# Performance work log

Measured on AMD Instinct MI355X. Metric: run time of the kernel, lower is better.

The kernel has to match this reference:

```python
import jax, jax.numpy as jnp
import numpy as np

N_QUBITS = 12
N_LAYERS = 2
PATCH = 16
NPS = 14  # patches per side for 224/16
N_PATCHES = NPS * NPS
SCALE = 1.0 / np.sqrt(N_QUBITS)


def _butterfly_gates(n):
    # Faithful replication of QuantumOrthogonalLayer.butterfly_circuit indexing:
    # param_idx increments even when the (idx1, idx2) pair is skipped.
    gates, pidx = [], 0
    n_bl = int(np.ceil(np.log2(n)))
    for layer in range(n_bl):
        stride = 2 ** layer
        for start in range(0, n - stride, 2 * stride):
            for off in range(stride):
                i1, i2 = start + off, start + off + stride
                if i1 < n and i2 < n:
                    gates.append((pidx, i1, i2))
                pidx += 1
    nppl = sum(2 ** (n_bl - 1 - i) * 2 ** i for i in range(n_bl))  # n_params() = 32
    return gates, nppl

GATES, NPPL = _butterfly_gates(N_QUBITS)

# Pauli-Z sign table: qubit 0 is the most-significant bit of the flattened state index.
_bits = (np.arange(2 ** N_QUBITS)[:, None] >> np.arange(N_QUBITS - 1, -1, -1)[None, :]) & 1
Z_SIGNS = jnp.asarray(1.0 - 2.0 * _bits, dtype=jnp.float32)  # (4096, 12)


def _rbs_u(theta):
    # 4x4 real unitary of RY(2t,w1); CNOT(w1,w2); RY(-2t,w1); CNOT(w1,w2)
    c, s = jnp.cos(theta), jnp.sin(theta)
    c2, s2, cs = c * c, s * s, c * s
    return jnp.stack([
        jnp.stack([c2, s2, -cs, cs]),
        jnp.stack([s2, c2, cs, -cs]),
        jnp.stack([cs, -cs, c2, s2]),
        jnp.stack([-cs, cs, s2, c2]),
    ])


def _apply_2q(state, U, i, j):
    # state: (P, 2, 2, ..., 2); apply U to qubit axes i, j
    st = jnp.moveaxis(state, (1 + i, 1 + j), (-2, -1))
    shp = st.shape
    st = st.reshape(shp[:-2] + (4,)) @ U.T
    return jnp.moveaxis(st.reshape(shp), (-2, -1), (1 + i, 1 + j))


@jax.checkpoint
def quantum_expvals(features, params):
    # features: (P, n_qubits) angles; params: (N_LAYERS * NPPL,)
    P = features.shape[0]
    half = 0.5 * features
    amp = jnp.stack([jnp.cos(half), jnp.sin(half)], axis=-1)  # (P, n, 2) RY(x)|0>
    state = jnp.ones((P, 1), features.dtype)
    for q in range(N_QUBITS):  # product-state angle encoding
        state = (state[:, :, None] * amp[:, q][:, None, :]).reshape(P, -1)
    state = state.reshape((P,) + (2,) * N_QUBITS)
    for l in range(N_LAYERS):
        base = l * NPPL
        for pidx, w1, w2 in GATES:
            state = _apply_2q(state, _rbs_u(params[base + pidx]), w1, w2)
    probs = state.reshape(P, -1) ** 2
    return probs @ Z_SIGNS  # (P, n_qubits) <Z_i>


def setup_inputs() -> dict:
    key = jax.random.key(0)
    ks = jax.random.split(key, 6)
    x = jax.random.normal(ks[0], (4, 3, 224, 224), dtype=jnp.float32)
    W_proj = jax.random.normal(ks[1], (N_QUBITS, PATCH * PATCH), dtype=jnp.float32) / np.sqrt(PATCH * PATCH)
    b_proj = jnp.zeros((N_QUBITS,), jnp.float32)
    q_params = 0.1 * jax.random.normal(ks[2], (N_LAYERS * NPPL,), dtype=jnp.float32)
    k_params = 0.1 * jax.random.normal(ks[3], (N_LAYERS * NPPL,), dtype=jnp.float32)
    v_params = 0.1 * jax.random.normal(ks[4], (N_LAYERS * NPPL,), dtype=jnp.float32)
    W_cls = jax.random.normal(ks[5], (1000, N_PATCHES * N_QUBITS), dtype=jnp.float32) / np.sqrt(N_PATCHES * N_QUBITS)
    b_cls = jnp.zeros((1000,), jnp.float32)
    return {"x": x, "W_proj": W_proj, "b_proj": b_proj, "q_params": q_params,
            "k_params": k_params, "v_params": v_params, "W_cls": W_cls, "b_cls": b_cls}


def reference(x, W_proj, b_proj, q_params, k_params, v_params, W_cls, b_cls):
    B = x.shape[0]
    xg = jnp.mean(x, axis=1)  # channel average -> (B, H, W)
    patches = xg.reshape(B, NPS, PATCH, NPS, PATCH).transpose(0, 1, 3, 2, 4)
    patches = patches.reshape(B, N_PATCHES, PATCH * PATCH)
    proj = patches @ W_proj.T + b_proj  # (B, n_patches, n_qubits)
    feats = proj.reshape(-1, N_QUBITS)
    Q = quantum_expvals(feats, q_params).reshape(B, N_PATCHES, N_QUBITS)
    K = quantum_expvals(feats, k_params).reshape(B, N_PATCHES, N_QUBITS)
    V = quantum_expvals(feats, v_params).reshape(B, N_PATCHES, N_QUBITS)
    attn = jax.nn.softmax(jnp.einsum('bqd,bkd->bqk', Q, K) * SCALE, axis=-1)
    out = jnp.einsum('bqk,bkd->bqd', attn, V)  # (B, n_patches, n_qubits)
    logits = out.reshape(B, -1) @ W_cls.T + b_cls
    return logits
```

## Files before the change

kernel.cpp:

```cpp
#include <hip/hip_runtime.h>
#include <math.h>

#define NQ        12
#define NPS       14
#define NPATCH    196
#define NB        4
#define NCLS      1000
#define FEATDIM   2352
#define SCALE_F   0.28867513459481287f
#define LSTRIDE   33

constexpr int PR[6][5] = {
    {11,10, 9, 8, 7},
    { 7, 6, 5, 4, 3},
    { 3, 2, 1, 0,11},
    {11,10, 7, 6, 3},
    {10, 9, 5, 2, 1},
    { 9, 8, 4, 1, 0},
};
constexpr int PT[6][7] = {
    { 5, 4, 3, 1, 2, 0, 6},
    {11,10, 2, 1, 9, 8, 0},
    { 8, 7, 6, 9, 5, 4,10},
    { 5, 8, 2, 1, 0, 4, 9},
    {11, 7, 8, 4, 6, 3, 0},
    { 5, 3,10, 7, 6, 2,11},
};

constexpr int wgt(int X, int pos) {
    for (int k = 0; k < 5; ++k) if (PR[X][k] == pos) return 1 << k;
    for (int k = 0; k < 7; ++k) if (PT[X][k] == pos) return LSTRIDE << k;
    return 0;
}
constexpr int rimm(int X, int Y, int r) {
    int s = 0;
    for (int j = 0; j < 5; ++j) if ((r >> j) & 1) s += wgt(X, PR[Y][j]);
    return s;
}

template<int X, int Y>
__device__ __forceinline__ void relayout(float amp[32], float* lds, int tid) {
    float* w = lds + LSTRIDE * tid;
    #pragma unroll
    for (int r = 0; r < 32; ++r) w[r] = amp[r];
    __syncthreads();
    int base = 0;
    #pragma unroll
    for (int j = 0; j < 7; ++j)
        base += ((tid >> j) & 1) ? wgt(X, PT[Y][j]) : 0;
    #pragma unroll
    for (int r = 0; r < 32; ++r)
        amp[r] = lds[base + rimm(X, Y, r)];
    __syncthreads();
}

template<int MI, int MJ>
__device__ __forceinline__ void apply_gate(float amp[32], float gc, float gs) {
    #pragma unroll
    for (int m = 0; m < 32; ++m) {
        if (m & (MI | MJ)) continue;
        float a0 = amp[m], a1 = amp[m | MJ], a2 = amp[m | MI], a3 = amp[m | MI | MJ];
        float p  = a0 + a1, q  = a0 - a1;
        float p2 = a2 + a3, q2 = a2 - a3;
        float t1 = 0.5f * p  + gc * q  - gs * q2;
        float t2 = 0.5f * p2 + gc * q2 + gs * q;
        amp[m]           = t1;
        amp[m | MJ]      = p  - t1;
        amp[m | MI]      = t2;
        amp[m | MI | MJ] = p2 - t2;
    }
}

__device__ const int SLOT[12] = {0,3,7,8,4,5,1,9,2,6,10,11};

__global__ __launch_bounds__(128, 4) void qcirc_kernel(
    const float* __restrict__ x,
    const float* __restrict__ Wp,
    const float* __restrict__ bproj,
    const float* __restrict__ qp,
    const float* __restrict__ kp,
    const float* __restrict__ vp,
    float* __restrict__ qkv)
{
    __shared__ __align__(16) float lds[128 * LSTRIDE];
    __shared__ float chs[NQ], shs[NQ];
    __shared__ float gC[40], gS[40];
    __shared__ float red2[2][12];

    const int tid = threadIdx.x;
    const int p = blockIdx.x, b = blockIdx.y, c = blockIdx.z;
    const int bp = b * NPATCH + p;
    const float* params = (c == 0) ? qp : (c == 1) ? kp : vp;

    float part[NQ];
    #pragma unroll
    for (int q = 0; q < NQ; ++q) part[q] = 0.0f;
    {
        int py = p / NPS, px = p % NPS;
        const float* xb = x + (size_t)b * 3 * 224 * 224;
        #pragma unroll
        for (int k = 0; k < 2; ++k) {
            int pix = tid + 128 * k;
            int off = (py * 16 + (pix >> 4)) * 224 + px * 16 + (pix & 15);
            float v = (xb[off] + xb[off + 50176] + xb[off + 100352]) * (1.0f / 3.0f);
            #pragma unroll
            for (int q = 0; q < NQ; ++q) part[q] += v * Wp[q * 256 + pix];
        }
    }
    if (tid < 40) {
        int l = tid / 20, g = tid - l * 20;
        float th = params[l * 32 + g];
        gC[tid] = 0.5f * cosf(2.0f * th);
        gS[tid] = 0.5f * sinf(2.0f * th);
    }
    #pragma unroll
    for (int o = 1; o < 64; o <<= 1) {
        #pragma unroll
        for (int q = 0; q < NQ; ++q) part[q] += __shfl_xor(part[q], o);
    }
    {
        int lane = tid & 63, wv = tid >> 6;
        if (lane == 0) {
            #pragma unroll
            for (int q = 0; q < NQ; ++q) red2[wv][q] = part[q];
        }
    }
    __syncthreads();
    if (tid < NQ) {
        float h = 0.5f * (red2[0][tid] + red2[1][tid] + bproj[tid]);
        chs[tid] = cosf(h); shs[tid] = sinf(h);
    }
    __syncthreads();

    float amp[32];
    {
        float hi = ((tid &  1) ? shs[6]  : chs[6])  *
                   ((tid &  2) ? shs[7]  : chs[7])  *
                   ((tid &  4) ? shs[8]  : chs[8])  *
                   ((tid &  8) ? shs[10] : chs[10]) *
                   ((tid & 16) ? shs[9]  : chs[9])  *
                   ((tid & 32) ? shs[11] : chs[11]) *
                   ((tid & 64) ? shs[5]  : chs[5]);
        float pA[8], pB[4];
        #pragma unroll
        for (int i = 0; i < 8; ++i)
            pA[i] = ((i & 1) ? shs[0] : chs[0]) * ((i & 2) ? shs[1] : chs[1]) *
                    ((i & 4) ? shs[2] : chs[2]);
        #pragma unroll
        for (int i = 0; i < 4; ++i)
            pB[i] = ((i & 1) ? shs[3] : chs[3]) * ((i & 2) ? shs[4] : chs[4]);
        #pragma unroll
        for (int r = 0; r < 32; ++r) amp[r] = pA[r & 7] * pB[r >> 3] * hi;
    }

    #pragma unroll 1
    for (int l = 0; l < 2; ++l) {
        const int bb = l * 20;
        apply_gate<1, 2>(amp, gC[bb+0], gS[bb+0]);
        apply_gate<4, 8>(amp, gC[bb+1], gS[bb+1]);
        apply_gate<1, 4>(amp, gC[bb+6], gS[bb+6]);
        apply_gate<2, 8>(amp, gC[bb+7], gS[bb+7]);
        relayout<0,1>(amp, lds, tid);
        apply_gate<1, 2>(amp, gC[bb+2], gS[bb+2]);
        apply_gate<4, 8>(amp, gC[bb+3], gS[bb+3]);
        apply_gate<1, 4>(amp, gC[bb+8], gS[bb+8]);
        apply_gate<2, 8>(amp, gC[bb+9], gS[bb+9]);
        relayout<1,2>(amp, lds, tid);
        apply_gate<1, 2>(amp, gC[bb+4],  gS[bb+4]);
        apply_gate<4, 8>(amp, gC[bb+5],  gS[bb+5]);
        apply_gate<1, 4>(amp, gC[bb+10], gS[bb+10]);
        apply_gate<2, 8>(amp, gC[bb+11], gS[bb+11]);
        relayout<2,3>(amp, lds, tid);
        apply_gate<1, 4>(amp, gC[bb+12], gS[bb+12]);
        apply_gate<2, 8>(amp, gC[bb+13], gS[bb+13]);
        apply_gate<1,16>(amp, gC[bb+16], gS[bb+16]);
        relayout<3,4>(amp, lds, tid);
        apply_gate<2, 4>(amp, gC[bb+14], gS[bb+14]);
        apply_gate<1, 8>(amp, gC[bb+17], gS[bb+17]);
        relayout<4,5>(amp, lds, tid);
        apply_gate<2, 4>(amp, gC[bb+15], gS[bb+15]);
        apply_gate<1, 8>(amp, gC[bb+18], gS[bb+18]);
        apply_gate<2,16>(amp, gC[bb+19], gS[bb+19]);
        if (l == 0) relayout<5,0>(amp, lds, tid);
    }

    float T, Sq2, Sq3, Sq7, Sq10, Sq11;
    {
        float t1[16]; Sq2 = 0.0f;
        #pragma unroll
        for (int i = 0; i < 16; ++i) {
            float e = amp[2*i] * amp[2*i], o = amp[2*i+1] * amp[2*i+1];
            t1[i] = e + o; Sq2 += e - o;
        }
        float t2[8]; Sq3 = 0.0f;
        #pragma unroll
        for (int i = 0; i < 8; ++i) { t2[i] = t1[2*i] + t1[2*i+1]; Sq3 += t1[2*i] - t1[2*i+1]; }
        float t3[4]; Sq7 = 0.0f;
        #pragma unroll
        for (int i = 0; i < 4; ++i) { t3[i] = t2[2*i] + t2[2*i+1]; Sq7 += t2[2*i] - t2[2*i+1]; }
        float t4[2]; Sq10 = 0.0f;
        #pragma unroll
        for (int i = 0; i < 2; ++i) { t4[i] = t3[2*i] + t3[2*i+1]; Sq10 += t3[2*i] - t3[2*i+1]; }
        T = t4[0] + t4[1]; Sq11 = t4[0] - t4[1];
    }
    float A = T, M[6];
    #pragma unroll
    for (int pbit = 0; pbit < 6; ++pbit) {
        int msk = 1 << pbit;
        float Ap = __shfl_xor(A, msk);
        float d  = A - Ap;
        M[pbit] = (tid & msk) ? -d : d;
        A += Ap;
        #pragma unroll
        for (int k = 0; k < 6; ++k)
            if (k < pbit) M[k] += __shfl_xor(M[k], msk);
        Sq2  += __shfl_xor(Sq2,  msk);
        Sq3  += __shfl_xor(Sq3,  msk);
        Sq7  += __shfl_xor(Sq7,  msk);
        Sq10 += __shfl_xor(Sq10, msk);
        Sq11 += __shfl_xor(Sq11, msk);
    }
    {
        int lane = tid & 63, wv = tid >> 6;
        if (lane == 0) {
            red2[wv][0] = A;
            red2[wv][1] = M[0];
            red2[wv][2] = M[1];
            red2[wv][3] = M[2];
            red2[wv][4] = M[3];
            red2[wv][5] = M[4];
            red2[wv][6] = M[5];
            red2[wv][7] = Sq2;  red2[wv][8]  = Sq3;
            red2[wv][9] = Sq7;  red2[wv][10] = Sq10; red2[wv][11] = Sq11;
        }
    }
    __syncthreads();
    if (tid < NQ) {
        int sl = SLOT[tid];
        float v0 = red2[0][sl], v1 = red2[1][sl];
        float s = (tid == 0) ? (v0 - v1) : (v0 + v1);
        qkv[((size_t)c * (NB * NPATCH) + bp) * NQ + tid] = s;
    }
}

__global__ __launch_bounds__(256) void attn_kernel(
    const float* __restrict__ qkv,
    float* __restrict__ outb)
{
    int tid = threadIdx.x;
    int qp = blockIdx.x, b = blockIdx.y;
    const float* Q = qkv;
    const float* K = qkv + NB * NPATCH * NQ;
    const float* V = qkv + 2 * NB * NPATCH * NQ;

    __shared__ float redm[4], reds[4], redv[4][NQ];

    float4 q0 = ((const float4*)(Q + (b * NPATCH + qp) * NQ))[0];
    float4 q1 = ((const float4*)(Q + (b * NPATCH + qp) * NQ))[1];
    float4 q2 = ((const float4*)(Q + (b * NPATCH + qp) * NQ))[2];

    float score = -1e30f;
    float4 v0, v1, v2;
    if (tid < NPATCH) {
        const float4* K4 = (const float4*)(K + (b * NPATCH + tid) * NQ);
        float4 k0 = K4[0], k1 = K4[1], k2 = K4[2];
        float s = q0.x*k0.x + q0.y*k0.y + q0.z*k0.z + q0.w*k0.w
                + q1.x*k1.x + q1.y*k1.y + q1.z*k1.z + q1.w*k1.w
                + q2.x*k2.x + q2.y*k2.y + q2.z*k2.z + q2.w*k2.w;
        score = s * SCALE_F;
        const float4* V4 = (const float4*)(V + (b * NPATCH + tid) * NQ);
        v0 = V4[0]; v1 = V4[1]; v2 = V4[2];
    }
    float m = score;
    #pragma unroll
    for (int o = 32; o > 0; o >>= 1) m = fmaxf(m, __shfl_down(m, o));
    int lane = tid & 63, wv = tid >> 6;
    if (lane == 0) redm[wv] = m;
    __syncthreads();
    float maxv = fmaxf(fmaxf(redm[0], redm[1]), fmaxf(redm[2], redm[3]));

    float w = (tid < NPATCH) ? expf(score - maxv) : 0.0f;
    float sm = w;
    #pragma unroll
    for (int o = 32; o > 0; o >>= 1) sm += __shfl_down(sm, o);
    if (lane == 0) reds[wv] = sm;

    float part[NQ];
    #pragma unroll
    for (int d = 0; d < NQ; d++) part[d] = 0.0f;
    if (tid < NPATCH) {
        part[0] = w*v0.x; part[1] = w*v0.y; part[2]  = w*v0.z; part[3]  = w*v0.w;
        part[4] = w*v1.x; part[5] = w*v1.y; part[6]  = w*v1.z; part[7]  = w*v1.w;
        part[8] = w*v2.x; part[9] = w*v2.y; part[10] = w*v2.z; part[11] = w*v2.w;
    }
    #pragma unroll
    for (int d = 0; d < NQ; d++) {
        #pragma unroll
        for (int o = 32; o > 0; o >>= 1) part[d] += __shfl_down(part[d], o);
    }
    if (lane == 0) {
        #pragma unroll
        for (int d = 0; d < NQ; d++) redv[wv][d] = part[d];
    }
    __syncthreads();
    if (tid < NQ) {
        float sumv = reds[0] + reds[1] + reds[2] + reds[3];
        float s = redv[0][tid] + redv[1][tid] + redv[2][tid] + redv[3][tid];
        outb[(size_t)b * FEATDIM + qp * NQ + tid] = s / sumv;
    }
}

__global__ __launch_bounds__(256) void cls_kernel(
    const float* __restrict__ outb,
    const float* __restrict__ Wc,
    const float* __restrict__ bc,
    float* __restrict__ logits)
{
    int o = blockIdx.x, tid = threadIdx.x;
    float acc[NB] = {0.0f, 0.0f, 0.0f, 0.0f};
    const float4* w4 = (const float4*)(Wc + (size_t)o * FEATDIM);
    for (int j = tid; j < FEATDIM / 4; j += 256) {
        float4 w = w4[j];
        #pragma unroll
        for (int b = 0; b < NB; b++) {
            float4 ov = ((const float4*)(outb + (size_t)b * FEATDIM))[j];
            acc[b] += w.x*ov.x + w.y*ov.y + w.z*ov.z + w.w*ov.w;
        }
    }
    #pragma unroll
    for (int b = 0; b < NB; b++) {
        #pragma unroll
        for (int off = 32; off > 0; off >>= 1) acc[b] += __shfl_down(acc[b], off);
    }
    __shared__ float red[4][NB];
    int lane = tid & 63, wv = tid >> 6;
    if (lane == 0) {
        #pragma unroll
        for (int b = 0; b < NB; b++) red[wv][b] = acc[b];
    }
    __syncthreads();
    if (tid < NB) {
        float s = red[0][tid] + red[1][tid] + red[2][tid] + red[3][tid];
        logits[(size_t)tid * NCLS + o] = s + bc[o];
    }
}

extern "C" void kernel_launch(void* const* d_in, const int* in_sizes, int n_in,
                              void* d_out, int out_size, void* d_ws, size_t ws_size,
                              hipStream_t stream) {
    const float* x     = (const float*)d_in[0];
    const float* Wp    = (const float*)d_in[1];
    const float* bproj = (const float*)d_in[2];
    const float* qp    = (const float*)d_in[3];
    const float* kp    = (const float*)d_in[4];
    const float* vp    = (const float*)d_in[5];
    const float* Wc    = (const float*)d_in[6];
    const float* bc    = (const float*)d_in[7];
    float* logits = (float*)d_out;

    float* ws   = (float*)d_ws;
    float* qkv  = ws;
    float* outb = ws + 28224;

    qcirc_kernel<<<dim3(NPATCH, NB, 3), 128, 0, stream>>>(x, Wp, bproj, qp, kp, vp, qkv);
    attn_kernel <<<dim3(NPATCH, NB),    256, 0, stream>>>(qkv, outb);
    cls_kernel  <<<NCLS,                256, 0, stream>>>(outb, Wc, bc, logits);
}
```

Baseline: 125.6 us.

## Split state-vector relayout into two half-size LDS passes to cut shared memory

The qubit relayout through LDS now moves the 32 per-thread amplitudes in two halves of 16 with a stride-17 buffer, instead of one 32-wide pass with stride 33. This roughly halves the LDS footprint, and launch bounds go from 4 to 5 blocks per CU to use that for occupancy. The qubit permutation tables, the initial product-state mapping and the output slot and sign mapping are redesigned so that each relayout keeps one local bit fixed. The cost is twice as many barriers and LDS round trips per relayout, plus 16 extra temporary registers.

New measurement: 125.0 us. About the same (-0.5%).

```diff
diff --git a/kernel.cpp b/kernel.cpp
--- a/kernel.cpp
+++ b/kernel.cpp
@@ -8,9 +8,8 @@
 #define NCLS      1000
 #define FEATDIM   2352
 #define SCALE_F   0.28867513459481287f
-#define LSTRIDE   33
-
-constexpr int PR[6][5] = {
+
+constexpr int PRa[6][5] = {
     {11,10, 9, 8, 7},
     { 7, 6, 5, 4, 3},
     { 3, 2, 1, 0,11},
@@ -18,40 +17,67 @@
     {10, 9, 5, 2, 1},
     { 9, 8, 4, 1, 0},
 };
-constexpr int PT[6][7] = {
-    { 5, 4, 3, 1, 2, 0, 6},
-    {11,10, 2, 1, 9, 8, 0},
-    { 8, 7, 6, 9, 5, 4,10},
-    { 5, 8, 2, 1, 0, 4, 9},
-    {11, 7, 8, 4, 6, 3, 0},
-    { 5, 3,10, 7, 6, 2,11},
+constexpr int PTa[6][7] = {
+    { 6, 5, 4, 3, 1, 0, 2},
+    {11,10, 1, 0, 9, 8, 2},
+    { 8, 9, 7, 6, 5, 4,10},
+    { 8, 5, 2, 1, 0, 4, 9},
+    { 7, 4, 0,11, 6, 3, 8},
+    { 6,11,10, 2, 5, 3, 7},
 };
-
-constexpr int wgt(int X, int pos) {
-    for (int k = 0; k < 5; ++k) if (PR[X][k] == pos) return 1 << k;
-    for (int k = 0; k < 7; ++k) if (PT[X][k] == pos) return LSTRIDE << k;
+constexpr int IXa[6] = {4,4,4,1,1,0};
+constexpr int IYa[6] = {0,0,0,0,0,2};
+
+constexpr int cwgt(int X, int IX, int pos) {
+    for (int k = 0; k < 5; ++k)
+        if (PRa[X][k] == pos) return (k == IX) ? 0 : (1 << (k - (k > IX ? 1 : 0)));
+    for (int m = 0; m < 7; ++m)
+        if (PTa[X][m] == pos) return 17 << m;
     return 0;
 }
-constexpr int rimm(int X, int Y, int r) {
+constexpr int rimm2(int X, int IX, int Y, int IY, int rc) {
     int s = 0;
-    for (int j = 0; j < 5; ++j) if ((r >> j) & 1) s += wgt(X, PR[Y][j]);
+    for (int j = 0; j < 4; ++j)
+        if ((rc >> j) & 1) s += cwgt(X, IX, PRa[Y][j + (j >= IY ? 1 : 0)]);
     return s;
 }
 
-template<int X, int Y>
-__device__ __forceinline__ void relayout(float amp[32], float* lds, int tid) {
-    float* w = lds + LSTRIDE * tid;
-    #pragma unroll
-    for (int r = 0; r < 32; ++r) w[r] = amp[r];
+template<int TI>
+__device__ __forceinline__ void relayout2(float amp[32], float* lds, int tid) {
+    constexpr int X = TI, Y = (TI + 1) % 6;
+    constexpr int IX = IXa[TI], IY = IYa[TI];
+    float tmp[16];
+    #pragma unroll
+    for (int rc = 0; rc < 16; ++rc) {
+        int r = (rc & ((1 << IX) - 1)) | ((rc >> IX) << (IX + 1));
+        lds[17 * tid + rc] = amp[r];
+    }
     __syncthreads();
     int base = 0;
     #pragma unroll
     for (int j = 0; j < 7; ++j)
-        base += ((tid >> j) & 1) ? wgt(X, PT[Y][j]) : 0;
-    #pragma unroll
-    for (int r = 0; r < 32; ++r)
-        amp[r] = lds[base + rimm(X, Y, r)];
-    __syncthreads();
+        base += ((tid >> j) & 1) ? cwgt(X, IX, PTa[Y][j]) : 0;
+    #pragma unroll
+    for (int rc = 0; rc < 16; ++rc)
+        tmp[rc] = lds[base + rimm2(X, IX, Y, IY, rc)];
+    __syncthreads();
+    #pragma unroll
+    for (int rc = 0; rc < 16; ++rc) {
+        int r = (rc & ((1 << IX) - 1)) | ((rc >> IX) << (IX + 1)) | (1 << IX);
+        lds[17 * tid + rc] = amp[r];
+    }
+    __syncthreads();
+    #pragma unroll
+    for (int rc = 0; rc < 16; ++rc) {
+        int r = (rc & ((1 << IY) - 1)) | ((rc >> IY) << (IY + 1)) | (1 << IY);
+        amp[r] = lds[base + rimm2(X, IX, Y, IY, rc)];
+    }
+    __syncthreads();
+    #pragma unroll
+    for (int rc = 0; rc < 16; ++rc) {
+        int r = (rc & ((1 << IY) - 1)) | ((rc >> IY) << (IY + 1));
+        amp[r] = tmp[rc];
+    }
 }
 
 template<int MI, int MJ>
@@ -71,9 +97,9 @@
     }
 }
 
-__device__ const int SLOT[12] = {0,3,7,8,4,5,1,9,2,6,10,11};
-
-__global__ __launch_bounds__(128, 4) void qcirc_kernel(
+__device__ const int SLOT[12] = {2,3,7,8,0,1,5,9,6,4,10,11};
+
+__global__ __launch_bounds__(128, 5) void qcirc_kernel(
     const float* __restrict__ x,
     const float* __restrict__ Wp,
     const float* __restrict__ bproj,
@@ -82,7 +108,7 @@
     const float* __restrict__ vp,
     float* __restrict__ qkv)
 {
-    __shared__ __align__(16) float lds[128 * LSTRIDE];
+    __shared__ __align__(16) float lds[2176];
     __shared__ float chs[NQ], shs[NQ];
     __shared__ float gC[40], gS[40];
     __shared__ float red2[2][12];
@@ -134,13 +160,13 @@
 
     float amp[32];
     {
-        float hi = ((tid &  1) ? shs[6]  : chs[6])  *
-                   ((tid &  2) ? shs[7]  : chs[7])  *
-                   ((tid &  4) ? shs[8]  : chs[8])  *
-                   ((tid &  8) ? shs[10] : chs[10]) *
-                   ((tid & 16) ? shs[9]  : chs[9])  *
+        float hi = ((tid &  1) ? shs[5]  : chs[5])  *
+                   ((tid &  2) ? shs[6]  : chs[6])  *
+                   ((tid &  4) ? shs[7]  : chs[7])  *
+                   ((tid &  8) ? shs[8]  : chs[8])  *
+                   ((tid & 16) ? shs[10] : chs[10]) *
                    ((tid & 32) ? shs[11] : chs[11]) *
-                   ((tid & 64) ? shs[5]  : chs[5]);
+                   ((tid & 64) ? shs[9]  : chs[9]);
         float pA[8], pB[4];
         #pragma unroll
         for (int i = 0; i < 8; ++i)
@@ -160,28 +186,28 @@
         apply_gate<4, 8>(amp, gC[bb+1], gS[bb+1]);
         apply_gate<1, 4>(amp, gC[bb+6], gS[bb+6]);
         apply_gate<2, 8>(amp, gC[bb+7], gS[bb+7]);
-        relayout<0,1>(amp, lds, tid);
+        relayout2<0>(amp, lds, tid);
         apply_gate<1, 2>(amp, gC[bb+2], gS[bb+2]);
         apply_gate<4, 8>(amp, gC[bb+3], gS[bb+3]);
         apply_gate<1, 4>(amp, gC[bb+8], gS[bb+8]);
         apply_gate<2, 8>(amp, gC[bb+9], gS[bb+9]);
-        relayout<1,2>(amp, lds, tid);
+        relayout2<1>(amp, lds, tid);
         apply_gate<1, 2>(amp, gC[bb+4],  gS[bb+4]);
         apply_gate<4, 8>(amp, gC[bb+5],  gS[bb+5]);
         apply_gate<1, 4>(amp, gC[bb+10], gS[bb+10]);
         apply_gate<2, 8>(amp, gC[bb+11], gS[bb+11]);
-        relayout<2,3>(amp, lds, tid);
+        relayout2<2>(amp, lds, tid);
         apply_gate<1, 4>(amp, gC[bb+12], gS[bb+12]);
         apply_gate<2, 8>(amp, gC[bb+13], gS[bb+13]);
         apply_gate<1,16>(amp, gC[bb+16], gS[bb+16]);
-        relayout<3,4>(amp, lds, tid);
+        relayout2<3>(amp, lds, tid);
         apply_gate<2, 4>(amp, gC[bb+14], gS[bb+14]);
         apply_gate<1, 8>(amp, gC[bb+17], gS[bb+17]);
-        relayout<4,5>(amp, lds, tid);
+        relayout2<4>(amp, lds, tid);
         apply_gate<2, 4>(amp, gC[bb+15], gS[bb+15]);
         apply_gate<1, 8>(amp, gC[bb+18], gS[bb+18]);
         apply_gate<2,16>(amp, gC[bb+19], gS[bb+19]);
-        if (l == 0) relayout<5,0>(amp, lds, tid);
+        if (l == 0) relayout2<5>(amp, lds, tid);
     }
 
     float T, Sq2, Sq3, Sq7, Sq10, Sq11;
@@ -224,12 +250,8 @@
         int lane = tid & 63, wv = tid >> 6;
         if (lane == 0) {
             red2[wv][0] = A;
-            red2[wv][1] = M[0];
-            red2[wv][2] = M[1];
-            red2[wv][3] = M[2];
-            red2[wv][4] = M[3];
-            red2[wv][5] = M[4];
-            red2[wv][6] = M[5];
+            red2[wv][1] = M[0]; red2[wv][2] = M[1]; red2[wv][3] = M[2];
+            red2[wv][4] = M[3]; red2[wv][5] = M[4]; red2[wv][6] = M[5];
             red2[wv][7] = Sq2;  red2[wv][8]  = Sq3;
             red2[wv][9] = Sq7;  red2[wv][10] = Sq10; red2[wv][11] = Sq11;
         }
@@ -238,7 +260,7 @@
     if (tid < NQ) {
         int sl = SLOT[tid];
         float v0 = red2[0][sl], v1 = red2[1][sl];
-        float s = (tid == 0) ? (v0 - v1) : (v0 + v1);
+        float s = (tid == 4) ? (v0 - v1) : (v0 + v1);
         qkv[((size_t)c * (NB * NPATCH) + bp) * NQ + tid] = s;
     }
 }
```

## Split LDS relayouts into halves, avoid block barriers, use DPP wave reductions

Applied to the files above, without the earlier changes.

Each qubit relayout now exchanges amplitudes through a smaller LDS buffer in two 16-element halves. Qubit assignments are chosen so that most exchanges stay within a wavefront, so those steps wait only on the LDS counter instead of a full __syncthreads. The shuffle-based butterfly reductions for the projection and the expectation values are replaced by DPP row/broadcast wave sums, and the per-qubit sign masks are applied before the reduction. This aims to cut barrier and shuffle overhead in the statevector kernel, but it relies on intra-wave LDS ordering being correct and makes the qubit bookkeeping more intricate.

Result: faster. 120.2 us (-4.3%).

```diff
diff --git a/kernel.cpp b/kernel.cpp
--- a/kernel.cpp
+++ b/kernel.cpp
@@ -8,50 +8,71 @@
 #define NCLS      1000
 #define FEATDIM   2352
 #define SCALE_F   0.28867513459481287f
-#define LSTRIDE   33
-
-constexpr int PR[6][5] = {
-    {11,10, 9, 8, 7},
-    { 7, 6, 5, 4, 3},
-    { 3, 2, 1, 0,11},
-    {11,10, 7, 6, 3},
-    {10, 9, 5, 2, 1},
-    { 9, 8, 4, 1, 0},
+
+constexpr int PRa[6][5] = {
+    { 0, 1, 2, 3, 4},
+    { 4, 5, 6, 7, 8},
+    { 9,10,11, 0, 8},
+    { 0, 4, 5, 8, 1},
+    { 1, 6, 9,10, 2},
+    { 7,10,11, 2, 3},
 };
-constexpr int PT[6][7] = {
-    { 5, 4, 3, 1, 2, 0, 6},
-    {11,10, 2, 1, 9, 8, 0},
-    { 8, 7, 6, 9, 5, 4,10},
-    { 5, 8, 2, 1, 0, 4, 9},
-    {11, 7, 8, 4, 6, 3, 0},
-    { 5, 3,10, 7, 6, 2,11},
+constexpr int PTa[6][7] = {
+    {10, 5, 6, 7,11, 8, 9},
+    { 1, 0, 3,10, 2,11, 9},
+    { 2, 1, 4, 6, 7, 5, 3},
+    { 7, 2, 6, 9,11,10, 3},
+    { 0, 7, 4, 5, 8,11, 3},
+    { 5, 0, 1, 6, 8, 4, 9},
 };
-
-constexpr int wgt(int X, int pos) {
-    for (int k = 0; k < 5; ++k) if (PR[X][k] == pos) return 1 << k;
-    for (int k = 0; k < 7; ++k) if (PT[X][k] == pos) return LSTRIDE << k;
+constexpr int  IYa[6]  = {0, 4, 3, 0, 3, 3};
+constexpr bool BARa[6] = {false, true, false, false, true, false};
+
+constexpr int cwgt(int X, int q) {
+    for (int k = 0; k < 4; ++k) if (PRa[X][k] == q) return 1 << k;
+    for (int m = 0; m < 7; ++m) if (PTa[X][m] == q) return 17 << m;
     return 0;
 }
-constexpr int rimm(int X, int Y, int r) {
+constexpr int rimm3(int X, int Y, int IY, int rc) {
     int s = 0;
-    for (int j = 0; j < 5; ++j) if ((r >> j) & 1) s += wgt(X, PR[Y][j]);
+    for (int j = 0; j < 4; ++j)
+        if ((rc >> j) & 1) s += cwgt(X, PRa[Y][j + (j >= IY ? 1 : 0)]);
     return s;
 }
-
-template<int X, int Y>
-__device__ __forceinline__ void relayout(float amp[32], float* lds, int tid) {
-    float* w = lds + LSTRIDE * tid;
-    #pragma unroll
-    for (int r = 0; r < 32; ++r) w[r] = amp[r];
-    __syncthreads();
+constexpr int expand(int rc, int IY) {
+    return (rc & ((1 << IY) - 1)) | ((rc >> IY) << (IY + 1));
+}
+
+__device__ __forceinline__ void wait_lgkm() {
+    __asm__ __volatile__("s_waitcnt lgkmcnt(0)" ::: "memory");
+}
+
+template<int TI>
+__device__ __forceinline__ void relayout3(float amp[32], float* lds, int tid) {
+    constexpr int X = TI, Y = (TI + 1) % 6, IY = IYa[TI];
+    constexpr bool BAR = BARa[TI];
+    float* w = lds + 17 * tid;
+    #pragma unroll
+    for (int rc = 0; rc < 16; ++rc) w[rc] = amp[rc];
+    if (BAR) __syncthreads(); else wait_lgkm();
     int base = 0;
     #pragma unroll
     for (int j = 0; j < 7; ++j)
-        base += ((tid >> j) & 1) ? wgt(X, PT[Y][j]) : 0;
-    #pragma unroll
-    for (int r = 0; r < 32; ++r)
-        amp[r] = lds[base + rimm(X, Y, r)];
-    __syncthreads();
+        base += ((tid >> j) & 1) ? cwgt(X, PTa[Y][j]) : 0;
+    float tmp[16];
+    #pragma unroll
+    for (int rc = 0; rc < 16; ++rc)
+        tmp[rc] = lds[base + rimm3(X, Y, IY, rc)];
+    if (BAR) __syncthreads(); else wait_lgkm();
+    #pragma unroll
+    for (int rc = 0; rc < 16; ++rc) w[rc] = amp[16 + rc];
+    if (BAR) __syncthreads(); else wait_lgkm();
+    #pragma unroll
+    for (int rc = 0; rc < 16; ++rc)
+        amp[expand(rc, IY) | (1 << IY)] = lds[base + rimm3(X, Y, IY, rc)];
+    if (BAR) __syncthreads();
+    #pragma unroll
+    for (int rc = 0; rc < 16; ++rc) amp[expand(rc, IY)] = tmp[rc];
 }
 
 template<int MI, int MJ>
@@ -71,7 +92,20 @@
     }
 }
 
-__device__ const int SLOT[12] = {0,3,7,8,4,5,1,9,2,6,10,11};
+template<int CTRL>
+__device__ __forceinline__ float dppadd(float x) {
+    int s = __builtin_amdgcn_update_dpp(0, __float_as_int(x), CTRL, 0xf, 0xf, true);
+    return x + __int_as_float(s);
+}
+__device__ __forceinline__ float wave_sum(float x) {
+    x = dppadd<0x111>(x);
+    x = dppadd<0x112>(x);
+    x = dppadd<0x114>(x);
+    x = dppadd<0x118>(x);
+    x = dppadd<0x142>(x);
+    x = dppadd<0x143>(x);
+    return x;
+}
 
 __global__ __launch_bounds__(128, 4) void qcirc_kernel(
     const float* __restrict__ x,
@@ -82,7 +116,7 @@
     const float* __restrict__ vp,
     float* __restrict__ qkv)
 {
-    __shared__ __align__(16) float lds[128 * LSTRIDE];
+    __shared__ __align__(16) float lds[2176];
     __shared__ float chs[NQ], shs[NQ];
     __shared__ float gC[40], gS[40];
     __shared__ float red2[2][12];
@@ -91,6 +125,7 @@
     const int p = blockIdx.x, b = blockIdx.y, c = blockIdx.z;
     const int bp = b * NPATCH + p;
     const float* params = (c == 0) ? qp : (c == 1) ? kp : vp;
+    const int lane = tid & 63, wv = tid >> 6;
 
     float part[NQ];
     #pragma unroll
@@ -114,16 +149,10 @@
         gS[tid] = 0.5f * sinf(2.0f * th);
     }
     #pragma unroll
-    for (int o = 1; o < 64; o <<= 1) {
-        #pragma unroll
-        for (int q = 0; q < NQ; ++q) part[q] += __shfl_xor(part[q], o);
-    }
-    {
-        int lane = tid & 63, wv = tid >> 6;
-        if (lane == 0) {
-            #pragma unroll
-            for (int q = 0; q < NQ; ++q) red2[wv][q] = part[q];
-        }
+    for (int q = 0; q < NQ; ++q) part[q] = wave_sum(part[q]);
+    if (lane == 63) {
+        #pragma unroll
+        for (int q = 0; q < NQ; ++q) red2[wv][q] = part[q];
     }
     __syncthreads();
     if (tid < NQ) {
@@ -134,13 +163,13 @@
 
     float amp[32];
     {
-        float hi = ((tid &  1) ? shs[6]  : chs[6])  *
-                   ((tid &  2) ? shs[7]  : chs[7])  *
-                   ((tid &  4) ? shs[8]  : chs[8])  *
-                   ((tid &  8) ? shs[10] : chs[10]) *
-                   ((tid & 16) ? shs[9]  : chs[9])  *
-                   ((tid & 32) ? shs[11] : chs[11]) *
-                   ((tid & 64) ? shs[5]  : chs[5]);
+        float hi = ((tid &  1) ? shs[10] : chs[10]) *
+                   ((tid &  2) ? shs[5]  : chs[5])  *
+                   ((tid &  4) ? shs[6]  : chs[6])  *
+                   ((tid &  8) ? shs[7]  : chs[7])  *
+                   ((tid & 16) ? shs[11] : chs[11]) *
+                   ((tid & 32) ? shs[8]  : chs[8])  *
+                   ((tid & 64) ? shs[9]  : chs[9]);
         float pA[8], pB[4];
         #pragma unroll
         for (int i = 0; i < 8; ++i)
@@ -160,85 +189,70 @@
         apply_gate<4, 8>(amp, gC[bb+1], gS[bb+1]);
         apply_gate<1, 4>(amp, gC[bb+6], gS[bb+6]);
         apply_gate<2, 8>(amp, gC[bb+7], gS[bb+7]);
-        relayout<0,1>(amp, lds, tid);
+        relayout3<0>(amp, lds, tid);
         apply_gate<1, 2>(amp, gC[bb+2], gS[bb+2]);
         apply_gate<4, 8>(amp, gC[bb+3], gS[bb+3]);
         apply_gate<1, 4>(amp, gC[bb+8], gS[bb+8]);
         apply_gate<2, 8>(amp, gC[bb+9], gS[bb+9]);
-        relayout<1,2>(amp, lds, tid);
-        apply_gate<1, 2>(amp, gC[bb+4],  gS[bb+4]);
-        apply_gate<4, 8>(amp, gC[bb+5],  gS[bb+5]);
-        apply_gate<1, 4>(amp, gC[bb+10], gS[bb+10]);
-        apply_gate<2, 8>(amp, gC[bb+11], gS[bb+11]);
-        relayout<2,3>(amp, lds, tid);
-        apply_gate<1, 4>(amp, gC[bb+12], gS[bb+12]);
-        apply_gate<2, 8>(amp, gC[bb+13], gS[bb+13]);
-        apply_gate<1,16>(amp, gC[bb+16], gS[bb+16]);
-        relayout<3,4>(amp, lds, tid);
-        apply_gate<2, 4>(amp, gC[bb+14], gS[bb+14]);
-        apply_gate<1, 8>(amp, gC[bb+17], gS[bb+17]);
-        relayout<4,5>(amp, lds, tid);
-        apply_gate<2, 4>(amp, gC[bb+15], gS[bb+15]);
-        apply_gate<1, 8>(amp, gC[bb+18], gS[bb+18]);
-        apply_gate<2,16>(amp, gC[bb+19], gS[bb+19]);
-        if (l == 0) relayout<5,0>(amp, lds, tid);
-    }
-
-    float T, Sq2, Sq3, Sq7, Sq10, Sq11;
+        relayout3<1>(amp, lds, tid);
+        apply_gate<16,1>(amp, gC[bb+4],  gS[bb+4]);
+        apply_gate<2, 4>(amp, gC[bb+5],  gS[bb+5]);
+        apply_gate<16,2>(amp, gC[bb+10], gS[bb+10]);
+        apply_gate<1, 4>(amp, gC[bb+11], gS[bb+11]);
+        relayout3<2>(amp, lds, tid);
+        apply_gate<1, 2>(amp, gC[bb+12], gS[bb+12]);
+        apply_gate<16,4>(amp, gC[bb+13], gS[bb+13]);
+        apply_gate<1, 8>(amp, gC[bb+16], gS[bb+16]);
+        relayout3<3>(amp, lds, tid);
+        apply_gate<16,2>(amp, gC[bb+14], gS[bb+14]);
+        apply_gate<1, 4>(amp, gC[bb+17], gS[bb+17]);
+        relayout3<4>(amp, lds, tid);
+        apply_gate<16,1>(amp, gC[bb+15], gS[bb+15]);
+        apply_gate<8, 2>(amp, gC[bb+18], gS[bb+18]);
+        apply_gate<16,4>(amp, gC[bb+19], gS[bb+19]);
+        if (l == 0) relayout3<5>(amp, lds, tid);
+    }
+
+    float T, Sq7, Sq10, Sq11, Sq2, Sq3;
     {
-        float t1[16]; Sq2 = 0.0f;
+        float t1[16]; Sq7 = 0.0f;
         #pragma unroll
         for (int i = 0; i < 16; ++i) {
             float e = amp[2*i] * amp[2*i], o = amp[2*i+1] * amp[2*i+1];
-            t1[i] = e + o; Sq2 += e - o;
+            t1[i] = e + o; Sq7 += e - o;
         }
-        float t2[8]; Sq3 = 0.0f;
-        #pragma unroll
-        for (int i = 0; i < 8; ++i) { t2[i] = t1[2*i] + t1[2*i+1]; Sq3 += t1[2*i] - t1[2*i+1]; }
-        float t3[4]; Sq7 = 0.0f;
-        #pragma unroll
-        for (int i = 0; i < 4; ++i) { t3[i] = t2[2*i] + t2[2*i+1]; Sq7 += t2[2*i] - t2[2*i+1]; }
-        float t4[2]; Sq10 = 0.0f;
-        #pragma unroll
-        for (int i = 0; i < 2; ++i) { t4[i] = t3[2*i] + t3[2*i+1]; Sq10 += t3[2*i] - t3[2*i+1]; }
-        T = t4[0] + t4[1]; Sq11 = t4[0] - t4[1];
-    }
-    float A = T, M[6];
-    #pragma unroll
-    for (int pbit = 0; pbit < 6; ++pbit) {
-        int msk = 1 << pbit;
-        float Ap = __shfl_xor(A, msk);
-        float d  = A - Ap;
-        M[pbit] = (tid & msk) ? -d : d;
-        A += Ap;
-        #pragma unroll
-        for (int k = 0; k < 6; ++k)
-            if (k < pbit) M[k] += __shfl_xor(M[k], msk);
-        Sq2  += __shfl_xor(Sq2,  msk);
-        Sq3  += __shfl_xor(Sq3,  msk);
-        Sq7  += __shfl_xor(Sq7,  msk);
-        Sq10 += __shfl_xor(Sq10, msk);
-        Sq11 += __shfl_xor(Sq11, msk);
-    }
-    {
-        int lane = tid & 63, wv = tid >> 6;
-        if (lane == 0) {
-            red2[wv][0] = A;
-            red2[wv][1] = M[0];
-            red2[wv][2] = M[1];
-            red2[wv][3] = M[2];
-            red2[wv][4] = M[3];
-            red2[wv][5] = M[4];
-            red2[wv][6] = M[5];
-            red2[wv][7] = Sq2;  red2[wv][8]  = Sq3;
-            red2[wv][9] = Sq7;  red2[wv][10] = Sq10; red2[wv][11] = Sq11;
-        }
+        float t2[8]; Sq10 = 0.0f;
+        #pragma unroll
+        for (int i = 0; i < 8; ++i) { t2[i] = t1[2*i] + t1[2*i+1]; Sq10 += t1[2*i] - t1[2*i+1]; }
+        float t3[4]; Sq11 = 0.0f;
+        #pragma unroll
+        for (int i = 0; i < 4; ++i) { t3[i] = t2[2*i] + t2[2*i+1]; Sq11 += t2[2*i] - t2[2*i+1]; }
+        float t4[2]; Sq2 = 0.0f;
+        #pragma unroll
+        for (int i = 0; i < 2; ++i) { t4[i] = t3[2*i] + t3[2*i+1]; Sq2 += t3[2*i] - t3[2*i+1]; }
+        T = t4[0] + t4[1]; Sq3 = t4[0] - t4[1];
+    }
+    float Vq5 = (tid &  1) ? -T : T;
+    float Vq0 = (tid &  2) ? -T : T;
+    float Vq1 = (tid &  4) ? -T : T;
+    float Vq6 = (tid &  8) ? -T : T;
+    float Vq8 = (tid & 16) ? -T : T;
+    float Vq4 = (tid & 32) ? -T : T;
+    T    = wave_sum(T);
+    Vq5  = wave_sum(Vq5);  Vq0  = wave_sum(Vq0);  Vq1  = wave_sum(Vq1);
+    Vq6  = wave_sum(Vq6);  Vq8  = wave_sum(Vq8);  Vq4  = wave_sum(Vq4);
+    Sq7  = wave_sum(Sq7);  Sq10 = wave_sum(Sq10); Sq11 = wave_sum(Sq11);
+    Sq2  = wave_sum(Sq2);  Sq3  = wave_sum(Sq3);
+    if (lane == 63) {
+        red2[wv][0]  = Vq0;  red2[wv][1]  = Vq1;  red2[wv][2]  = Sq2;
+        red2[wv][3]  = Sq3;  red2[wv][4]  = Vq4;  red2[wv][5]  = Vq5;
+        red2[wv][6]  = Vq6;  red2[wv][7]  = Sq7;  red2[wv][8]  = Vq8;
+        red2[wv][9]  = T;    red2[wv][10] = Sq10; red2[wv][11] = Sq11;
     }
     __syncthreads();
     if (tid < NQ) {
-        int sl = SLOT[tid];
-        float v0 = red2[0][sl], v1 = red2[1][sl];
-        float s = (tid == 0) ? (v0 - v1) : (v0 + v1);
+        float v1 = red2[1][tid];
+        float s = red2[0][tid] + ((tid == 9) ? -v1 : v1);
         qkv[((size_t)c * (NB * NPATCH) + bp) * NQ + tid] = s;
     }
 }
```
